# Performance work log

Measured on AMD Instinct MI355X. Metric: run time of the kernel, lower is better.

The kernel has to match this reference:

```python
import jax, jax.numpy as jnp
import numpy as np
from jax import lax

WIN_SIZE = 11
SIGMA = 1.5
CHANNELS = 3
C1 = (0.01 * 255) ** 2
C2 = (0.03 * 255) ** 2


def fspecial_gauss(size, sigma, channels):
    x, y = np.mgrid[-size // 2 + 1:size // 2 + 1, -size // 2 + 1:size // 2 + 1]
    g = np.exp(-((x ** 2 + y ** 2) / (2.0 * sigma ** 2)))
    g = (g / g.sum()).astype(np.float32)
    # depthwise kernel, OIHW with I=1, O=channels
    return jnp.asarray(np.tile(g[None, None], (channels, 1, 1, 1)))


def _gauss_filter(x, win):
    # depthwise valid conv, NCHW
    return lax.conv_general_dilated(
        x, win, window_strides=(1, 1), padding='VALID',
        feature_group_count=x.shape[1],
        dimension_numbers=('NCHW', 'OIHW', 'NCHW'))


def setup_inputs() -> dict:
    key = jax.random.key(0)
    k1, k2 = jax.random.split(key)
    X = jax.random.uniform(k1, (32, 3, 512, 512), dtype=jnp.float32)
    Y = jax.random.uniform(k2, (32, 3, 512, 512), dtype=jnp.float32)
    win = fspecial_gauss(WIN_SIZE, SIGMA, CHANNELS)
    return {"X": X, "Y": Y, "win": win}


def reference(X, Y, win):
    mu1 = _gauss_filter(X, win)
    mu2 = _gauss_filter(Y, win)
    mu1_sq = mu1 * mu1
    mu2_sq = mu2 * mu2
    mu1_mu2 = mu1 * mu2
    sigma1_sq = _gauss_filter(X * X, win) - mu1_sq
    sigma2_sq = _gauss_filter(Y * Y, win) - mu2_sq
    sigma12 = _gauss_filter(X * Y, win) - mu1_mu2
    cs_map = jax.nn.relu((2 * sigma12 + C2) / (sigma1_sq + sigma2_sq + C2))
    ssim_map = (2 * mu1_mu2 + C1) / (mu1_sq + mu2_sq + C1) * cs_map
    ssim_val = jnp.mean(ssim_map, axis=(1, 2, 3))  # per-image SSIM
    return 1.0 - jnp.mean(ssim_val)  # as_loss=True
```

## Files before the change

### kernel.cpp

```cpp
#include <hip/hip_runtime.h>
#include <math.h>


#define WIN   11
#define IMG   512
#define OUT_N 502
#define TO_R  32
#define TO_C  64
#define TI_C  (TO_C + WIN - 1)
#define VB_W  77
#define NF    4
#define C1F   6.5025f
#define C2F   58.5225f
#define GRID_X 8
#define GRID_Y 16
#define GRID_Z 96

struct GaussW { float w[WIN]; };

template<bool CR, bool CC>
__device__ __forceinline__ void vert_task(
    const float* __restrict__ Xp, const float* __restrict__ Yp,
    const GaussW& gw, float (*vb)[TO_R][VB_W],
    int r0, int gc, int i0, int c)
{
    if (CC) gc = min(gc, IMG - 1);
    float a0[8] = {0}, a1[8] = {0}, a2[8] = {0}, a3[8] = {0};
#pragma unroll
    for (int k = 0; k < 18; ++k) {
        int gr = r0 + k;
        if (CR) gr = min(gr, IMG - 1);
        size_t off = (size_t)gr * IMG + gc;
        float x = Xp[off];
        float y = Yp[off];
        float s = x + y, d = x - y;
        float ss = s * s, dd = d * d;
        const int jlo = (k > 10) ? (k - 10) : 0;
        const int jhi = (k < 7) ? k : 7;
#pragma unroll
        for (int j = jlo; j <= jhi; ++j) {
            float wv = gw.w[k - j];
            a0[j] += wv * x;
            a1[j] += wv * y;
            a2[j] += wv * ss;
            a3[j] += wv * dd;
        }
    }
#pragma unroll
    for (int j = 0; j < 8; ++j) {
        int i = i0 + j;
        vb[0][i][c] = a0[j];
        vb[1][i][c] = a1[j];
        vb[2][i][c] = a2[j];
        vb[3][i][c] = a3[j];
    }
}

__global__ __launch_bounds__(256) void ssim_v8_kernel(
    const float* __restrict__ X, const float* __restrict__ Y,
    GaussW gw, double* __restrict__ acc)
{
    __shared__ float vb[NF][TO_R][VB_W];

    const int plane = blockIdx.z;
    const int ox0 = blockIdx.x * TO_C;
    const int oy0 = blockIdx.y * TO_R;
    const float* Xp = X + (size_t)plane * IMG * IMG;
    const float* Yp = Y + (size_t)plane * IMG * IMG;
    const int tid  = threadIdx.x;
    const int wave = tid >> 6;
    const int lane = tid & 63;

    {
        const int r0 = __builtin_amdgcn_readfirstlane(oy0 + wave * 8);
        const int gc = ox0 + lane;
        if (blockIdx.y == GRID_Y - 1)
            vert_task<true,  false>(Xp, Yp, gw, vb, r0, gc, wave * 8, lane);
        else
            vert_task<false, false>(Xp, Yp, gw, vb, r0, gc, wave * 8, lane);
    }
    if (wave == 0 && lane < 40) {
        const int s = lane / 10;
        const int c = TO_C + (lane - s * 10);
        vert_task<true, true>(Xp, Yp, gw, vb, oy0 + s * 8, ox0 + c, s * 8, c);
    }
    __syncthreads();

    const int i  = tid >> 3;
    const int c0 = (tid & 7) * 8;
    const int gi = oy0 + i;
    float m[NF][8];
#pragma unroll
    for (int f = 0; f < NF; ++f) {
        float v[18];
#pragma unroll
        for (int k = 0; k < 18; ++k) v[k] = vb[f][i][c0 + k];
#pragma unroll
        for (int oc = 0; oc < 8; ++oc) {
            float s = 0.f;
#pragma unroll
            for (int k = 0; k < WIN; ++k) s += gw.w[k] * v[oc + k];
            m[f][oc] = s;
        }
    }

    float psum = 0.f;
#pragma unroll
    for (int oc = 0; oc < 8; ++oc) {
        int gj = ox0 + c0 + oc;
        if (gi < OUT_N && gj < OUT_N) {
            float m1 = m[0][oc], m2 = m[1][oc];
            float P  = m[2][oc], M  = m[3][oc];
            float mu1s = m1 * m1, mu2s = m2 * m2, mu12 = m1 * m2;
            float sumvar = 0.5f  * (P + M) - mu1s - mu2s;
            float sig12  = 0.25f * (P - M) - mu12;
            float num = (2.f * mu12 + C1F) * (2.f * sig12 + C2F);
            float den = (mu1s + mu2s + C1F) * (sumvar + C2F);
            num = fmaxf(num, 0.f);
            psum += num * __builtin_amdgcn_rcpf(den);
        }
    }

#pragma unroll
    for (int off = 32; off > 0; off >>= 1)
        psum += __shfl_down(psum, off, 64);
    __shared__ float wsum[4];
    if ((tid & 63) == 0) wsum[tid >> 6] = psum;
    __syncthreads();
    if (tid == 0) {
        float s = wsum[0] + wsum[1] + wsum[2] + wsum[3];
        atomicAdd(acc, (double)s);
    }
}

__global__ void ssim_finalize_kernel(const double* __restrict__ acc,
                                     float* __restrict__ out)
{
    if (threadIdx.x == 0 && blockIdx.x == 0) {
        const double count = (double)GRID_Z * OUT_N * OUT_N;
        out[0] = (float)(1.0 - (*acc) / count);
    }
}

extern "C" void kernel_launch(void* const* d_in, const int* in_sizes, int n_in,
                              void* d_out, int out_size, void* d_ws, size_t ws_size,
                              hipStream_t stream) {
    (void)in_sizes; (void)n_in; (void)out_size; (void)ws_size;
    const float* X = (const float*)d_in[0];
    const float* Y = (const float*)d_in[1];
    float* out = (float*)d_out;
    double* acc = (double*)d_ws;

    hipMemsetAsync(d_ws, 0, sizeof(double), stream);

    GaussW gw;
    {
        double g[WIN], s = 0.0;
        for (int i = 0; i < WIN; ++i) {
            double d = (double)(i - 5);
            g[i] = exp(-(d * d) / (2.0 * 1.5 * 1.5));
            s += g[i];
        }
        for (int i = 0; i < WIN; ++i) gw.w[i] = (float)(g[i] / s);
    }

    dim3 grid(GRID_X, GRID_Y, GRID_Z);
    ssim_v8_kernel<<<grid, 256, 0, stream>>>(X, Y, gw, acc);
    ssim_finalize_kernel<<<1, 64, 0, stream>>>(acc, out);
}
```

Measured before the change: 319.3 us.

## Replace global double atomic and finalize kernel with hierarchical last-block reduction

New measurement: 291.1 us. 1.1x faster.

```diff
diff --git a/kernel.cpp b/kernel.cpp
--- a/kernel.cpp
+++ b/kernel.cpp
@@ -15,6 +15,7 @@
 #define GRID_X 8
 #define GRID_Y 16
 #define GRID_Z 96
+#define BLKS_PER_PLANE (GRID_X * GRID_Y)
 
 struct GaussW { float w[WIN]; };
 
@@ -56,10 +57,15 @@
     }
 }
 
-__global__ __launch_bounds__(256) void ssim_v8_kernel(
+__global__ __launch_bounds__(256) void ssim_v10_kernel(
     const float* __restrict__ X, const float* __restrict__ Y,
-    GaussW gw, double* __restrict__ acc)
+    GaussW gw, unsigned int* __restrict__ ws_u32, float* __restrict__ out)
 {
+    unsigned int* pctr     = ws_u32;
+    unsigned int* gctr     = ws_u32 + 96;
+    float*        planesum = (float*)(ws_u32 + 128);
+    float*        partial  = (float*)(ws_u32 + 256);
+
     __shared__ float vb[NF][TO_R][VB_W];
 
     const int plane = blockIdx.z;
@@ -127,18 +133,57 @@
     __shared__ float wsum[4];
     if ((tid & 63) == 0) wsum[tid >> 6] = psum;
     __syncthreads();
+
+    __shared__ int role;
     if (tid == 0) {
         float s = wsum[0] + wsum[1] + wsum[2] + wsum[3];
-        atomicAdd(acc, (double)s);
-    }
-}
-
-__global__ void ssim_finalize_kernel(const double* __restrict__ acc,
-                                     float* __restrict__ out)
-{
-    if (threadIdx.x == 0 && blockIdx.x == 0) {
-        const double count = (double)GRID_Z * OUT_N * OUT_N;
-        out[0] = (float)(1.0 - (*acc) / count);
+        const int pidx = plane * BLKS_PER_PLANE + blockIdx.y * GRID_X + blockIdx.x;
+        __hip_atomic_store(&partial[pidx], s, __ATOMIC_RELAXED,
+                           __HIP_MEMORY_SCOPE_AGENT);
+        asm volatile("s_waitcnt vmcnt(0)" ::: "memory");
+        unsigned old = __hip_atomic_fetch_add(&pctr[plane], 1u,
+                           __ATOMIC_RELAXED, __HIP_MEMORY_SCOPE_AGENT);
+        role = (old == BLKS_PER_PLANE - 1) ? 1 : 0;
+    }
+    __syncthreads();
+
+    if (role) {
+        float v = 0.f;
+        if (tid < BLKS_PER_PLANE)
+            v = __hip_atomic_load(&partial[plane * BLKS_PER_PLANE + tid],
+                                  __ATOMIC_RELAXED, __HIP_MEMORY_SCOPE_AGENT);
+#pragma unroll
+        for (int off = 32; off > 0; off >>= 1)
+            v += __shfl_down(v, off, 64);
+        if ((tid & 63) == 0) wsum[tid >> 6] = v;
+        __syncthreads();
+        if (tid == 0) {
+            float ps = wsum[0] + wsum[1] + wsum[2] + wsum[3];
+            __hip_atomic_store(&planesum[plane], ps, __ATOMIC_RELAXED,
+                               __HIP_MEMORY_SCOPE_AGENT);
+            asm volatile("s_waitcnt vmcnt(0)" ::: "memory");
+            unsigned o2 = __hip_atomic_fetch_add(gctr, 1u,
+                               __ATOMIC_RELAXED, __HIP_MEMORY_SCOPE_AGENT);
+            role = (o2 == GRID_Z - 1) ? 2 : 0;
+        }
+        __syncthreads();
+        if (role == 2) {
+            double v2 = 0.0;
+            if (tid < GRID_Z)
+                v2 = (double)__hip_atomic_load(&planesum[tid],
+                               __ATOMIC_RELAXED, __HIP_MEMORY_SCOPE_AGENT);
+#pragma unroll
+            for (int off = 32; off > 0; off >>= 1)
+                v2 += __shfl_down(v2, off, 64);
+            __shared__ double dsum[4];
+            if ((tid & 63) == 0) dsum[tid >> 6] = v2;
+            __syncthreads();
+            if (tid == 0) {
+                double a = dsum[0] + dsum[1] + dsum[2] + dsum[3];
+                const double count = (double)GRID_Z * OUT_N * OUT_N;
+                out[0] = (float)(1.0 - a / count);
+            }
+        }
     }
 }
 
@@ -149,9 +194,9 @@
     const float* X = (const float*)d_in[0];
     const float* Y = (const float*)d_in[1];
     float* out = (float*)d_out;
-    double* acc = (double*)d_ws;
-
-    hipMemsetAsync(d_ws, 0, sizeof(double), stream);
+    unsigned int* ws_u32 = (unsigned int*)d_ws;
+
+    hipMemsetAsync(d_ws, 0, 512, stream);
 
     GaussW gw;
     {
@@ -165,6 +210,5 @@
     }
 
     dim3 grid(GRID_X, GRID_Y, GRID_Z);
-    ssim_v8_kernel<<<grid, 256, 0, stream>>>(X, Y, gw, acc);
-    ssim_finalize_kernel<<<1, 64, 0, stream>>>(acc, out);
+    ssim_v10_kernel<<<grid, 256, 0, stream>>>(X, Y, gw, ws_u32, out);
 }
```
